# Performance work log

Hardware: AMD Instinct MI355X
Metric: run time of the kernel (lower is better)

Reference implementation:

```python
import jax, jax.numpy as jnp
import numpy as np

N = 1_000_000  # samples
G = 8          # groups of 3 binary variables; group g>=1 conditioned on group g-1


def _simplex_init(key, shape):
    # torch FactorizedDistribution.simplex_init: log of sorted-diff of uniforms
    t = jax.random.uniform(key, (int(np.prod(shape)),))
    t = t.at[-1].set(1.0)
    t = jnp.sort(t)
    t = jnp.concatenate([t[:1], t[1:] - t[:-1]])
    return jnp.log(t).reshape(shape)


def setup_inputs() -> dict:
    key = jax.random.key(0)
    k1, k2, k3, k4 = jax.random.split(key, 4)
    q0 = _simplex_init(k1, (2, 2, 2))                      # root group table
    qg = jnp.stack([_simplex_init(k, (2,) * 6)
                    for k in jax.random.split(k2, G - 1)])  # (G-1, 2,2,2, 2,2,2)
    # Gumbel noise -log(-log(U)) precomputed (torch draws it inside sample())
    u0 = jax.random.uniform(k3, (N, 2, 2, 2), minval=1e-10, maxval=1.0)
    ug = jax.random.uniform(k4, (G - 1, N, 2, 2, 2), minval=1e-10, maxval=1.0)
    noise0 = -jnp.log(-jnp.log(u0))
    noise = -jnp.log(-jnp.log(ug))
    return {"q0": q0, "qg": qg, "noise0": noise0, "noise": noise}


def _argmax_bits(gm):
    # flatten over the group's 2x2x2 cells, argmax, unravel to 3 bits
    n = gm.shape[0]
    idx = jnp.argmax(gm.reshape(n, -1), axis=1)            # (n,)
    return jnp.stack([(idx >> 2) & 1, (idx >> 1) & 1, idx & 1], axis=1)  # (n,3)


def reference(q0, qg, noise0, noise):
    # Group 0: unconditional Gumbel-max over (2,2,2) table
    gm = q0[None] + noise0                                  # (N,2,2,2)
    bits = _argmax_bits(gm)
    samples = [bits]
    # Groups 1..G-1: gather conditional slice with previous group's bits
    for g in range(qg.shape[0]):
        c = samples[-1]                                     # (N,3) int, values in {0,1}
        t = qg[g][c[:, 0], c[:, 1], c[:, 2]]                # (N,2,2,2) gathered slice
        bits = _argmax_bits(t + noise[g])
        samples.append(bits)
    return jnp.concatenate(samples, axis=1)                 # (N, G*3) sampled bits
```

## Files before the change

### kernel.cpp

```cpp
#include <hip/hip_runtime.h>


#define NGROUPS 8

__global__ __launch_bounds__(256) void fd_sample_kernel(
    const float* __restrict__ q0,
    const float* __restrict__ qg,
    const float* __restrict__ noise0,
    const float* __restrict__ noise,
    int* __restrict__ out,
    int N)
{
    const int i = blockIdx.x * blockDim.x + threadIdx.x;
    if (i >= N) return;

    float nz[NGROUPS][8];
    {
        const float4* p = (const float4*)noise0 + (size_t)i * 2;
        float4 a = p[0], b = p[1];
        nz[0][0] = a.x; nz[0][1] = a.y; nz[0][2] = a.z; nz[0][3] = a.w;
        nz[0][4] = b.x; nz[0][5] = b.y; nz[0][6] = b.z; nz[0][7] = b.w;
    }
#pragma unroll
    for (int g = 1; g < NGROUPS; ++g) {
        const float4* p = (const float4*)noise + ((size_t)(g - 1) * N + i) * 2;
        float4 a = p[0], b = p[1];
        nz[g][0] = a.x; nz[g][1] = a.y; nz[g][2] = a.z; nz[g][3] = a.w;
        nz[g][4] = b.x; nz[g][5] = b.y; nz[g][6] = b.z; nz[g][7] = b.w;
    }

    int idxs[NGROUPS];

    {
        int   best_i = 0;
        float best_v = q0[0] + nz[0][0];
#pragma unroll
        for (int k = 1; k < 8; ++k) {
            float v = q0[k] + nz[0][k];
            if (v > best_v) { best_v = v; best_i = k; }
        }
        idxs[0] = best_i;
    }

#pragma unroll
    for (int g = 1; g < NGROUPS; ++g) {
        const float4* tp = (const float4*)(qg + ((size_t)(g - 1) * 64 + (size_t)idxs[g - 1] * 8));
        float4 ta = tp[0], tb = tp[1];
        float t[8] = { ta.x, ta.y, ta.z, ta.w, tb.x, tb.y, tb.z, tb.w };

        int   best_i = 0;
        float best_v = t[0] + nz[g][0];
#pragma unroll
        for (int k = 1; k < 8; ++k) {
            float v = t[k] + nz[g][k];
            if (v > best_v) { best_v = v; best_i = k; }
        }
        idxs[g] = best_i;
    }

    int bits[24];
#pragma unroll
    for (int g = 0; g < NGROUPS; ++g) {
        bits[g * 3 + 0] = (idxs[g] >> 2) & 1;
        bits[g * 3 + 1] = (idxs[g] >> 1) & 1;
        bits[g * 3 + 2] = idxs[g] & 1;
    }
    int4* op = (int4*)out + (size_t)i * 6;
#pragma unroll
    for (int j = 0; j < 6; ++j)
        op[j] = make_int4(bits[j * 4 + 0], bits[j * 4 + 1], bits[j * 4 + 2], bits[j * 4 + 3]);
}

extern "C" void kernel_launch(void* const* d_in, const int* in_sizes, int n_in,
                              void* d_out, int out_size, void* d_ws, size_t ws_size,
                              hipStream_t stream) {
    const float* q0     = (const float*)d_in[0];
    const float* qg     = (const float*)d_in[1];
    const float* noise0 = (const float*)d_in[2];
    const float* noise  = (const float*)d_in[3];
    int* out = (int*)d_out;

    const int N = in_sizes[2] / 8;

    const int block = 256;
    const int grid  = (N + block - 1) / block;
    fd_sample_kernel<<<grid, block, 0, stream>>>(q0, qg, noise0, noise, out, N);
}
```

Before: 368.2 us.

## Stage tables and output in LDS, coalesce stores, and software-pipeline noise loads

Copies the conditional tables into shared memory so the data-dependent gathers hit LDS instead of global memory. Noise loads become rolling double-buffered: each group's next noise slice is fetched while the current group is reduced, which lowers register pressure and allows a higher occupancy hint. Output bits are packed into shared memory and written back as block-contiguous int4 stores so consecutive threads write adjacent addresses. The costs are two block barriers, extra LDS traffic, and fewer noise loads in flight per thread, since the prefetch now reaches only one group ahead.

```diff
diff --git a/kernel.cpp b/kernel.cpp
--- a/kernel.cpp
+++ b/kernel.cpp
@@ -3,7 +3,7 @@
 
 #define NGROUPS 8
 
-__global__ __launch_bounds__(256) void fd_sample_kernel(
+__global__ __launch_bounds__(256, 6) void fd_sample_kernel(
     const float* __restrict__ q0,
     const float* __restrict__ qg,
     const float* __restrict__ noise0,
@@ -11,64 +11,91 @@
     int* __restrict__ out,
     int N)
 {
-    const int i = blockIdx.x * blockDim.x + threadIdx.x;
-    if (i >= N) return;
+    __shared__ __align__(16) float s_tab[7 * 64];
+    __shared__ unsigned int s_out[256 * 7];
 
-    float nz[NGROUPS][8];
-    {
-        const float4* p = (const float4*)noise0 + (size_t)i * 2;
-        float4 a = p[0], b = p[1];
-        nz[0][0] = a.x; nz[0][1] = a.y; nz[0][2] = a.z; nz[0][3] = a.w;
-        nz[0][4] = b.x; nz[0][5] = b.y; nz[0][6] = b.z; nz[0][7] = b.w;
-    }
-#pragma unroll
-    for (int g = 1; g < NGROUPS; ++g) {
-        const float4* p = (const float4*)noise + ((size_t)(g - 1) * N + i) * 2;
-        float4 a = p[0], b = p[1];
-        nz[g][0] = a.x; nz[g][1] = a.y; nz[g][2] = a.z; nz[g][3] = a.w;
-        nz[g][4] = b.x; nz[g][5] = b.y; nz[g][6] = b.z; nz[g][7] = b.w;
-    }
+    const int t = threadIdx.x;
+
+    if (t < 112)
+        ((float4*)s_tab)[t] = ((const float4*)qg)[t];
+
+    const int  i      = blockIdx.x * blockDim.x + t;
+    const bool active = (i < N);
+    const int  ii     = active ? i : (N - 1);
+
+    const float4* p0 = (const float4*)noise0 + (size_t)ii * 2;
+    float4 ca = p0[0], cb = p0[1];
+    const float4* p1 = (const float4*)noise + (size_t)ii * 2;
+    float4 pa = p1[0], pb = p1[1];
 
     int idxs[NGROUPS];
 
     {
-        int   best_i = 0;
-        float best_v = q0[0] + nz[0][0];
+        float n[8] = {ca.x, ca.y, ca.z, ca.w, cb.x, cb.y, cb.z, cb.w};
+        float bv = q0[0] + n[0];
+        int   bi = 0;
 #pragma unroll
         for (int k = 1; k < 8; ++k) {
-            float v = q0[k] + nz[0][k];
-            if (v > best_v) { best_v = v; best_i = k; }
+            float v = q0[k] + n[k];
+            if (v > bv) { bv = v; bi = k; }
         }
-        idxs[0] = best_i;
+        idxs[0] = bi;
     }
+
+    __syncthreads();
 
 #pragma unroll
     for (int g = 1; g < NGROUPS; ++g) {
-        const float4* tp = (const float4*)(qg + ((size_t)(g - 1) * 64 + (size_t)idxs[g - 1] * 8));
+        ca = pa; cb = pb;
+        if (g < NGROUPS - 1) {
+            const float4* pn = (const float4*)noise + ((size_t)g * N + ii) * 2;
+            pa = pn[0]; pb = pn[1];
+        }
+        const float4* tp = (const float4*)(s_tab + (g - 1) * 64 + idxs[g - 1] * 8);
         float4 ta = tp[0], tb = tp[1];
-        float t[8] = { ta.x, ta.y, ta.z, ta.w, tb.x, tb.y, tb.z, tb.w };
+        float tt[8] = {ta.x, ta.y, ta.z, ta.w, tb.x, tb.y, tb.z, tb.w};
+        float nn[8] = {ca.x, ca.y, ca.z, ca.w, cb.x, cb.y, cb.z, cb.w};
 
-        int   best_i = 0;
-        float best_v = t[0] + nz[g][0];
+        float bv = tt[0] + nn[0];
+        int   bi = 0;
 #pragma unroll
         for (int k = 1; k < 8; ++k) {
-            float v = t[k] + nz[g][k];
-            if (v > best_v) { best_v = v; best_i = k; }
+            float v = tt[k] + nn[k];
+            if (v > bv) { bv = v; bi = k; }
         }
-        idxs[g] = best_i;
+        idxs[g] = bi;
     }
 
-    int bits[24];
+    {
+        unsigned int by[24];
 #pragma unroll
-    for (int g = 0; g < NGROUPS; ++g) {
-        bits[g * 3 + 0] = (idxs[g] >> 2) & 1;
-        bits[g * 3 + 1] = (idxs[g] >> 1) & 1;
-        bits[g * 3 + 2] = idxs[g] & 1;
+        for (int g = 0; g < NGROUPS; ++g) {
+            by[g * 3 + 0] = (idxs[g] >> 2) & 1;
+            by[g * 3 + 1] = (idxs[g] >> 1) & 1;
+            by[g * 3 + 2] = idxs[g] & 1;
+        }
+#pragma unroll
+        for (int d = 0; d < 6; ++d)
+            s_out[t * 7 + d] = by[4 * d] | (by[4 * d + 1] << 8) |
+                               (by[4 * d + 2] << 16) | (by[4 * d + 3] << 24);
     }
-    int4* op = (int4*)out + (size_t)i * 6;
+
+    __syncthreads();
+
+    const size_t block_i4 = (size_t)blockIdx.x * 1536;
 #pragma unroll
-    for (int j = 0; j < 6; ++j)
-        op[j] = make_int4(bits[j * 4 + 0], bits[j * 4 + 1], bits[j * 4 + 2], bits[j * 4 + 3]);
+    for (int j = 0; j < 6; ++j) {
+        int k = j * 256 + t;
+        int s = k / 6;
+        int e = k - s * 6;
+        unsigned int w  = s_out[s * 7 + e];
+        int gs = blockIdx.x * 256 + s;
+        if (gs < N) {
+            int4 o = make_int4((int)(w & 0xffu), (int)((w >> 8) & 0xffu),
+                               (int)((w >> 16) & 0xffu), (int)(w >> 24));
+            ((int4*)out)[block_i4 + k] = o;
+        }
+    }
 }
 
 extern "C" void kernel_launch(void* const* d_in, const int* in_sizes, int n_in,
```

Result: faster. 355.8 us (-3.4%).
